# Kernel optimization log

Measured on AMD Instinct MI355X. Metric: run time of the kernel, lower is better.

Reference implementation:

```python
import jax, jax.numpy as jnp
import numpy as np

B, S, E, H = 4, 2048, 1024, 16
D = E // H  # head_dim = 64
SCALE = D ** -0.5
THETA = 10000.0


def _rope_tables(seq_len, head_dim):
    half = head_dim // 2
    inv_freq = 1.0 / (THETA ** (jnp.arange(half, dtype=jnp.float32) / half))
    ang = jnp.arange(seq_len, dtype=jnp.float32)[:, None] * inv_freq[None, :]  # [S, D/2]
    ang = jnp.concatenate([ang, ang], axis=-1)  # [S, D]
    return jnp.cos(ang), jnp.sin(ang)


def setup_inputs() -> dict:
    key = jax.random.key(0)
    kx, kw, ko = jax.random.split(key, 3)
    x = jax.random.normal(kx, (B, S, E), dtype=jnp.float32)
    in_proj_weight = jax.random.normal(kw, (3 * E, E), dtype=jnp.float32) * (E ** -0.5)
    in_proj_bias = jnp.zeros((3 * E,), dtype=jnp.float32)
    out_w = jax.random.normal(ko, (E, E), dtype=jnp.float32) * (E ** -0.5)
    out_b = jnp.zeros((E,), dtype=jnp.float32)
    cos, sin = _rope_tables(S, D)
    return {"x": x, "in_proj_weight": in_proj_weight, "in_proj_bias": in_proj_bias,
            "out_w": out_w, "out_b": out_b, "cos": cos, "sin": sin}


def _rotate_half(t):
    t1, t2 = jnp.split(t, 2, axis=-1)
    return jnp.concatenate([-t2, t1], axis=-1)


def reference(x, in_proj_weight, in_proj_bias, out_w, out_b, cos, sin):
    b, s, e = x.shape
    # fused QKV projection: [b, s, 3E]
    proj = x @ in_proj_weight.T + in_proj_bias
    q, k, v = jnp.split(proj, 3, axis=-1)
    # b s (h d) -> b h s d
    to_heads = lambda t: t.reshape(b, s, H, D).transpose(0, 2, 1, 3)
    q, k, v = to_heads(q), to_heads(k), to_heads(v)
    # RoPE (rotate-half) on q, k; cos/sin: [S, D] broadcast over batch/heads
    c = cos[None, None, :, :]
    sn = sin[None, None, :, :]
    q = q * c + _rotate_half(q) * sn
    k = k * c + _rotate_half(k) * sn
    # SDPA, non-causal, explicit scale = head_dim**-0.5
    scores = jnp.einsum("bhqd,bhkd->bhqk", q, k) * SCALE
    attn = jax.nn.softmax(scores, axis=-1)
    o = jnp.einsum("bhqk,bhkd->bhqd", attn, v)
    # b h s d -> b s (h d)
    o = o.transpose(0, 2, 1, 3).reshape(b, s, e)
    return o @ out_w.T + out_b
```

## Files before the change

### kernel.cpp

```cpp
#include <hip/hip_runtime.h>

#define NB 4
#define NS 2048
#define NE 1024
#define NH 16
#define ND 64
#define KVB 64

typedef unsigned short ushort_t;
typedef __attribute__((ext_vector_type(8))) short bf16x8;
typedef __attribute__((ext_vector_type(4))) float f32x4;

#define SCALE_LOG2E 0.18033688011112042f

static __device__ __forceinline__ ushort_t f2bf(float f) {
    union { float f; unsigned int u; } v; v.f = f;
    unsigned int r = v.u + 0x7FFF + ((v.u >> 16) & 1);
    return (ushort_t)(r >> 16);
}

static __device__ __forceinline__ unsigned pk_bf16(float lo, float hi) {
    unsigned r;
    asm("v_cvt_pk_bf16_f32 %0, %1, %2" : "=v"(r) : "v"(lo), "v"(hi));
    return r;
}

static __device__ __forceinline__ void gload16(const void* g, void* l) {
    __builtin_amdgcn_global_load_lds(
        (const __attribute__((address_space(1))) void*)g,
        (__attribute__((address_space(3))) void*)l,
        16, 0, 0);
}

__global__ __launch_bounds__(256)
void cvt_f32_bf16(const float* __restrict__ src, ushort_t* __restrict__ dst, int n8)
{
    const int i = blockIdx.x * 256 + threadIdx.x;
    if (i >= n8) return;
    const float4 a = ((const float4*)src)[i * 2];
    const float4 b = ((const float4*)src)[i * 2 + 1];
    union { ushort_t us[8]; uint4 v; } pk;
    pk.us[0] = f2bf(a.x); pk.us[1] = f2bf(a.y); pk.us[2] = f2bf(a.z); pk.us[3] = f2bf(a.w);
    pk.us[4] = f2bf(b.x); pk.us[5] = f2bf(b.y); pk.us[6] = f2bf(b.z); pk.us[7] = f2bf(b.w);
    ((uint4*)dst)[i] = pk.v;
}

template<int EPI>
__global__ __launch_bounds__(256)
void gemm_bf16(const ushort_t* __restrict__ A, const ushort_t* __restrict__ W,
               const float* __restrict__ bias, float* __restrict__ C,
               ushort_t* __restrict__ Cb, int M, int N, int K)
{
    __shared__ ushort_t As[128 * 32];
    __shared__ ushort_t Bs[128 * 32];
    const int tid  = threadIdx.x;
    const int lane = tid & 63;
    const int wid  = tid >> 6;
    const int lr   = lane & 15;
    const int lg   = lane >> 4;
    const int m0 = blockIdx.y * 128;
    const int n0 = blockIdx.x * 128;
    const int wr = wid >> 1, wc = wid & 1;

    size_t srcoff[2];
    int ldsoff[2];
#pragma unroll
    for (int p = 0; p < 2; ++p) {
        const int chunk = p * 256 + tid;
        const int row = chunk >> 2;
        const int sp  = chunk & 3;
        const int c   = sp ^ ((row >> 1) & 3);
        srcoff[p] = (size_t)row * K + c * 8;
        ldsoff[p] = (p * 256 + wid * 64) * 8;
    }
    const ushort_t* Ag = A + (size_t)m0 * K;
    const ushort_t* Wg = W + (size_t)n0 * K;

    int offa[4], offb[4];
#pragma unroll
    for (int f = 0; f < 4; ++f) {
        const int ra = wr * 64 + f * 16 + lr;
        offa[f] = ra * 32 + (lg ^ ((ra >> 1) & 3)) * 8;
        const int rb = wc * 64 + f * 16 + lr;
        offb[f] = rb * 32 + (lg ^ ((rb >> 1) & 3)) * 8;
    }

    f32x4 acc[4][4];
#pragma unroll
    for (int i = 0; i < 4; ++i)
#pragma unroll
        for (int j = 0; j < 4; ++j) acc[i][j] = (f32x4){0.f, 0.f, 0.f, 0.f};

    for (int k0 = 0; k0 < K; k0 += 32) {
        __syncthreads();
#pragma unroll
        for (int p = 0; p < 2; ++p) {
            gload16(Ag + srcoff[p] + k0, (ushort_t*)As + ldsoff[p]);
            gload16(Wg + srcoff[p] + k0, (ushort_t*)Bs + ldsoff[p]);
        }
        __syncthreads();
        bf16x8 af[4], bfr[4];
#pragma unroll
        for (int f = 0; f < 4; ++f) {
            af[f]  = *(const bf16x8*)&As[offa[f]];
            bfr[f] = *(const bf16x8*)&Bs[offb[f]];
        }
#pragma unroll
        for (int mf = 0; mf < 4; ++mf)
#pragma unroll
            for (int nf = 0; nf < 4; ++nf)
                acc[mf][nf] = __builtin_amdgcn_mfma_f32_16x16x32_bf16(
                    af[mf], bfr[nf], acc[mf][nf], 0, 0, 0);
    }

    if (EPI == 0) {
#pragma unroll
        for (int nf = 0; nf < 4; ++nf) {
            const int n = n0 + wc * 64 + nf * 16 + lr;
            const float bj = bias[n];
#pragma unroll
            for (int mf = 0; mf < 4; ++mf)
#pragma unroll
                for (int r = 0; r < 4; ++r) {
                    const int m = m0 + wr * 64 + mf * 16 + lg * 4 + r;
                    C[(size_t)m * N + n] = acc[mf][nf][r] + bj;
                }
        }
    } else {
#pragma unroll
        for (int nf = 0; nf < 4; ++nf) {
            const int n = n0 + wc * 64 + nf * 16 + lr;
            const float bj = bias[n];
            const int t = n >> 10;
            const int h = (n >> 6) & (NH - 1);
            const int d = n & (ND - 1);
#pragma unroll
            for (int mf = 0; mf < 4; ++mf)
#pragma unroll
                for (int r = 0; r < 4; ++r) {
                    const int m = m0 + wr * 64 + mf * 16 + lg * 4 + r;
                    const int b = m >> 11;
                    const int s = m & (NS - 1);
                    Cb[((size_t)((t * NB + b) * NH + h) * NS + s) * ND + d] =
                        f2bf(acc[mf][nf][r] + bj);
                }
        }
    }
}

__global__ __launch_bounds__(256)
void rope_bf16(ushort_t* __restrict__ qkvb, const float* __restrict__ cosT,
               const float* __restrict__ sinT)
{
    const int idx = blockIdx.x * 256 + threadIdx.x;
    const int d0 = (idx & 3) * 8;
    const int s  = (idx >> 2) & (NS - 1);
    const int h  = (idx >> 13) & (NH - 1);
    const int b  = (idx >> 17) & (NB - 1);
    const int t  = idx >> 19;
    ushort_t* base = qkvb + ((size_t)((t * NB + b) * NH + h) * NS + s) * ND;

    union { ushort_t us[8]; uint4 v; } lo, hi, loo, hio;
    lo.v = *(const uint4*)(base + d0);
    hi.v = *(const uint4*)(base + d0 + 32);
    const float4 c0 = *(const float4*)(cosT + s * ND + d0);
    const float4 c1 = *(const float4*)(cosT + s * ND + d0 + 4);
    const float4 s0 = *(const float4*)(sinT + s * ND + d0);
    const float4 s1 = *(const float4*)(sinT + s * ND + d0 + 4);
    const float cc[8] = {c0.x, c0.y, c0.z, c0.w, c1.x, c1.y, c1.z, c1.w};
    const float ss[8] = {s0.x, s0.y, s0.z, s0.w, s1.x, s1.y, s1.z, s1.w};
#pragma unroll
    for (int j = 0; j < 8; ++j) {
        union { unsigned u; float f; } a, bb;
        a.u  = ((unsigned)lo.us[j]) << 16;
        bb.u = ((unsigned)hi.us[j]) << 16;
        loo.us[j] = f2bf(a.f * cc[j] - bb.f * ss[j]);
        hio.us[j] = f2bf(bb.f * cc[j] + a.f * ss[j]);
    }
    *(uint4*)(base + d0)      = loo.v;
    *(uint4*)(base + d0 + 32) = hio.v;
}

__global__ __launch_bounds__(256)
void attn_kernel(const ushort_t* __restrict__ qkvb, ushort_t* __restrict__ obuf)
{
    __shared__ ushort_t Ks[64 * 72];
    __shared__ ushort_t Vs[64 * 64];
    __shared__ ushort_t Ps[128 * 72];

    const int tid  = threadIdx.x;
    const int lane = tid & 63;
    const int wid  = tid >> 6;
    const int lr   = lane & 15;
    const int lg   = lane >> 4;

    const int orig = blockIdx.x;
    const int wg   = (orig & 7) * 128 + (orig >> 3);
    const int bh   = wg >> 4;
    const int b = bh >> 4, h = bh & (NH - 1);
    const int q0 = (wg & 15) * 128;

    const ushort_t* qbase = qkvb + ((size_t)((0 * NB + b) * NH + h)) * (NS * ND);
    const ushort_t* kbase = qkvb + ((size_t)((1 * NB + b) * NH + h)) * (NS * ND);
    const ushort_t* vbase = qkvb + ((size_t)((2 * NB + b) * NH + h)) * (NS * ND);

    bf16x8 qf[2][2];
#pragma unroll
    for (int st = 0; st < 2; ++st)
#pragma unroll
        for (int kh = 0; kh < 2; ++kh)
            qf[st][kh] = *(const bf16x8*)(qbase + (size_t)(q0 + wid * 32 + st * 16 + lr) * ND
                                          + kh * 32 + lg * 8);

    const int sc = tid & 7;
    const int sr0 = tid >> 3;

    uint4 krg[2], vrg[2];
#pragma unroll
    for (int it = 0; it < 2; ++it) {
        const int r = sr0 + it * 32;
        krg[it] = *(const uint4*)(kbase + r * ND + sc * 8);
        vrg[it] = *(const uint4*)(vbase + r * ND + sc * 8);
    }

    f32x4 acc_o[2][4];
    float lsum[2] = {0.f, 0.f};
#pragma unroll
    for (int st = 0; st < 2; ++st)
#pragma unroll
        for (int dk = 0; dk < 4; ++dk) acc_o[st][dk] = (f32x4){0.f, 0.f, 0.f, 0.f};

    for (int kt = 0; kt < NS; kt += KVB) {
        __syncthreads();
#pragma unroll
        for (int it = 0; it < 2; ++it) {
            const int r = sr0 + it * 32;
            *(uint4*)&Ks[r * 72 + sc * 8] = krg[it];
            union { uint4 v; ushort_t us[8]; } pu;
            pu.v = vrg[it];
#pragma unroll
            for (int j = 0; j < 8; ++j) {
                const int sw = (j ^ sc) << 4;
                Vs[(sc * 8 + j) * 64 + ((((r * 2) ^ sw)) >> 1)] = pu.us[j];
            }
        }
        __syncthreads();
        if (kt + KVB < NS) {
#pragma unroll
            for (int it = 0; it < 2; ++it) {
                const int r = kt + KVB + sr0 + it * 32;
                krg[it] = *(const uint4*)(kbase + (size_t)r * ND + sc * 8);
                vrg[it] = *(const uint4*)(vbase + (size_t)r * ND + sc * 8);
            }
        }

        f32x4 s[2][4];
#pragma unroll
        for (int st = 0; st < 2; ++st)
#pragma unroll
            for (int kvf = 0; kvf < 4; ++kvf) s[st][kvf] = (f32x4){0.f, 0.f, 0.f, 0.f};
        __builtin_amdgcn_s_setprio(1);
#pragma unroll
        for (int kh = 0; kh < 2; ++kh)
#pragma unroll
            for (int kvf = 0; kvf < 4; ++kvf) {
                const bf16x8 kf = *(const bf16x8*)&Ks[(kvf * 16 + lr) * 72 + kh * 32 + lg * 8];
                s[0][kvf] = __builtin_amdgcn_mfma_f32_16x16x32_bf16(kf, qf[0][kh], s[0][kvf], 0, 0, 0);
                s[1][kvf] = __builtin_amdgcn_mfma_f32_16x16x32_bf16(kf, qf[1][kh], s[1][kvf], 0, 0, 0);
            }
        __builtin_amdgcn_s_setprio(0);

#pragma unroll
        for (int st = 0; st < 2; ++st) {
            const int prow = (wid * 32 + st * 16 + lr) * 72;
#pragma unroll
            for (int kvf = 0; kvf < 4; ++kvf) {
                const float p0 = __builtin_amdgcn_exp2f(s[st][kvf][0] * SCALE_LOG2E);
                const float p1 = __builtin_amdgcn_exp2f(s[st][kvf][1] * SCALE_LOG2E);
                const float p2 = __builtin_amdgcn_exp2f(s[st][kvf][2] * SCALE_LOG2E);
                const float p3 = __builtin_amdgcn_exp2f(s[st][kvf][3] * SCALE_LOG2E);
                lsum[st] += (p0 + p1) + (p2 + p3);
                const unsigned w01 = pk_bf16(p0, p1);
                const unsigned w23 = pk_bf16(p2, p3);
                *(uint2*)&Ps[prow + kvf * 16 + lg * 4] = make_uint2(w01, w23);
            }
        }
        __syncthreads();

        __builtin_amdgcn_s_setprio(1);
#pragma unroll
        for (int kh = 0; kh < 2; ++kh) {
            const bf16x8 pf0 = *(const bf16x8*)&Ps[(wid * 32 + 0  + lr) * 72 + kh * 32 + lg * 8];
            const bf16x8 pf1 = *(const bf16x8*)&Ps[(wid * 32 + 16 + lr) * 72 + kh * 32 + lg * 8];
#pragma unroll
            for (int dk = 0; dk < 4; ++dk) {
                const int d = dk * 16 + lr;
                const int sw = ((d & 7) ^ ((d >> 3) & 7)) << 4;
                const bf16x8 vf = *(const bf16x8*)&Vs[d * 64 + (((kh * 64 + lg * 16) ^ sw) >> 1)];
                acc_o[0][dk] = __builtin_amdgcn_mfma_f32_16x16x32_bf16(pf0, vf, acc_o[0][dk], 0, 0, 0);
                acc_o[1][dk] = __builtin_amdgcn_mfma_f32_16x16x32_bf16(pf1, vf, acc_o[1][dk], 0, 0, 0);
            }
        }
        __builtin_amdgcn_s_setprio(0);
    }

#pragma unroll
    for (int st = 0; st < 2; ++st) {
        float r = lsum[st];
        r += __shfl_xor(r, 16);
        r += __shfl_xor(r, 32);
        float invq[4];
#pragma unroll
        for (int reg = 0; reg < 4; ++reg)
            invq[reg] = 1.0f / __shfl(r, lg * 4 + reg);
#pragma unroll
        for (int dk = 0; dk < 4; ++dk)
#pragma unroll
            for (int reg = 0; reg < 4; ++reg) {
                const int q = q0 + wid * 32 + st * 16 + lg * 4 + reg;
                const int d = dk * 16 + lr;
                obuf[((size_t)(b * NS + q)) * NE + h * ND + d] =
                    f2bf(acc_o[st][dk][reg] * invq[reg]);
            }
    }
}

extern "C" void kernel_launch(void* const* d_in, const int* in_sizes, int n_in,
                              void* d_out, int out_size, void* d_ws, size_t ws_size,
                              hipStream_t stream)
{
    const float* x    = (const float*)d_in[0];
    const float* Win  = (const float*)d_in[1];
    const float* bin  = (const float*)d_in[2];
    const float* Wout = (const float*)d_in[3];
    const float* bout = (const float*)d_in[4];
    const float* cosT = (const float*)d_in[5];
    const float* sinT = (const float*)d_in[6];
    float* out  = (float*)d_out;

    ushort_t* qkvb  = (ushort_t*)d_ws;
    ushort_t* obufb = qkvb + (size_t)3 * NB * NH * NS * ND;
    ushort_t* xb    = obufb + (size_t)NB * NS * NE;
    ushort_t* Wib   = xb + (size_t)NB * NS * NE;
    ushort_t* Wob   = Wib + (size_t)3 * NE * NE;

    const int nx = NB * NS * NE;
    const int nwi = 3 * NE * NE;
    const int nwo = NE * NE;

    cvt_f32_bf16<<<nx / 2048, 256, 0, stream>>>(x, xb, nx / 8);
    cvt_f32_bf16<<<nwi / 2048, 256, 0, stream>>>(Win, Wib, nwi / 8);
    cvt_f32_bf16<<<nwo / 2048, 256, 0, stream>>>(Wout, Wob, nwo / 8);

    gemm_bf16<1><<<dim3(3 * NE / 128, NB * NS / 128), 256, 0, stream>>>(
        xb, Wib, bin, nullptr, qkvb, NB * NS, 3 * NE, NE);
    rope_bf16<<<(2 * NB * NH * NS * 4) / 256, 256, 0, stream>>>(qkvb, cosT, sinT);
    attn_kernel<<<dim3(NB * NH * (NS / 128)), 256, 0, stream>>>(qkvb, obufb);
    gemm_bf16<0><<<dim3(NE / 128, NB * NS / 128), 256, 0, stream>>>(
        obufb, Wob, bout, out, nullptr, NB * NS, NE, NE);
}
```

Measured before the change: 258.7 us.

## Fuse convert launches, swizzle GEMM blocks across XCDs, drop attention block barrier

Replaces the three f32-to-bf16 conversion launches with one kernel that picks its source by block index, removing two launch overheads. The GEMM remaps linear block IDs so that consecutive tiles land on the same XCD, which should improve L2 reuse of A and W tiles. In attention, the __syncthreads between the P write and the P read becomes an LDS waitcnt plus a sched barrier. This is valid because each wave only reads back its own P rows, and it removes a workgroup-wide stall in every KV iteration.

```diff
diff --git a/kernel.cpp b/kernel.cpp
--- a/kernel.cpp
+++ b/kernel.cpp
@@ -33,10 +33,15 @@
 }
 
 __global__ __launch_bounds__(256)
-void cvt_f32_bf16(const float* __restrict__ src, ushort_t* __restrict__ dst, int n8)
-{
-    const int i = blockIdx.x * 256 + threadIdx.x;
-    if (i >= n8) return;
+void cvt3_f32_bf16(const float* __restrict__ x,  ushort_t* __restrict__ xb,
+                   const float* __restrict__ Wi, ushort_t* __restrict__ Wib,
+                   const float* __restrict__ Wo, ushort_t* __restrict__ Wob)
+{
+    const int blk = blockIdx.x;
+    const float* src; ushort_t* dst; int i;
+    if (blk < 4096)      { src = x;  dst = xb;  i = blk * 256 + threadIdx.x; }
+    else if (blk < 5632) { src = Wi; dst = Wib; i = (blk - 4096) * 256 + threadIdx.x; }
+    else                 { src = Wo; dst = Wob; i = (blk - 5632) * 256 + threadIdx.x; }
     const float4 a = ((const float4*)src)[i * 2];
     const float4 b = ((const float4*)src)[i * 2 + 1];
     union { ushort_t us[8]; uint4 v; } pk;
@@ -58,17 +63,23 @@
     const int wid  = tid >> 6;
     const int lr   = lane & 15;
     const int lg   = lane >> 4;
-    const int m0 = blockIdx.y * 128;
-    const int n0 = blockIdx.x * 128;
+
+    const int lin   = blockIdx.y * gridDim.x + blockIdx.x;
+    const int chunk = (gridDim.x * gridDim.y) >> 3;
+    const int lin2  = (lin & 7) * chunk + (lin >> 3);
+    const int bx    = lin2 % gridDim.x;
+    const int by    = lin2 / gridDim.x;
+    const int m0 = by * 128;
+    const int n0 = bx * 128;
     const int wr = wid >> 1, wc = wid & 1;
 
     size_t srcoff[2];
     int ldsoff[2];
 #pragma unroll
     for (int p = 0; p < 2; ++p) {
-        const int chunk = p * 256 + tid;
-        const int row = chunk >> 2;
-        const int sp  = chunk & 3;
+        const int chnk = p * 256 + tid;
+        const int row = chnk >> 2;
+        const int sp  = chnk & 3;
         const int c   = sp ^ ((row >> 1) & 3);
         srcoff[p] = (size_t)row * K + c * 8;
         ldsoff[p] = (p * 256 + wid * 64) * 8;
@@ -285,7 +296,8 @@
                 *(uint2*)&Ps[prow + kvf * 16 + lg * 4] = make_uint2(w01, w23);
             }
         }
-        __syncthreads();
+        asm volatile("s_waitcnt lgkmcnt(0)" ::: "memory");
+        __builtin_amdgcn_sched_barrier(0);
 
         __builtin_amdgcn_s_setprio(1);
 #pragma unroll
@@ -344,13 +356,7 @@
     ushort_t* Wib   = xb + (size_t)NB * NS * NE;
     ushort_t* Wob   = Wib + (size_t)3 * NE * NE;
 
-    const int nx = NB * NS * NE;
-    const int nwi = 3 * NE * NE;
-    const int nwo = NE * NE;
-
-    cvt_f32_bf16<<<nx / 2048, 256, 0, stream>>>(x, xb, nx / 8);
-    cvt_f32_bf16<<<nwi / 2048, 256, 0, stream>>>(Win, Wib, nwi / 8);
-    cvt_f32_bf16<<<nwo / 2048, 256, 0, stream>>>(Wout, Wob, nwo / 8);
+    cvt3_f32_bf16<<<6144, 256, 0, stream>>>(x, xb, Win, Wib, Wout, Wob);
 
     gemm_bf16<1><<<dim3(3 * NE / 128, NB * NS / 128), 256, 0, stream>>>(
         xb, Wib, bin, nullptr, qkvb, NB * NS, 3 * NE, NE);
```

After: 249.9 us. 1.04x faster.
